# Performance work log

Measured on AMD Instinct MI355X. Metric: run time of the kernel, lower is better.

## Reference

```python
import jax, jax.numpy as jnp
import numpy as np

BIG = 1e8   # fill value used by to_dense_batch for missing neighbors in the original
EPS_W = 1e-8
EPS_BN = 1e-5


def setup_inputs() -> dict:
    key = jax.random.key(0)
    ks = jax.random.split(key, 8)
    N, S, Dc, Df = 16384, 4096, 256, 64
    fine_xyz = jax.random.normal(ks[0], (1, 3, N), dtype=jnp.float32)
    coarse_xyz = jax.random.normal(ks[1], (1, 3, S), dtype=jnp.float32)
    fine_piece_id = jnp.sort(jax.random.randint(ks[2], (1, 1, N), 0, 4))
    coarse_piece_id = jnp.sort(jax.random.randint(ks[3], (1, 1, S), 0, 4))
    fine_features = jax.random.normal(ks[4], (1, Df, N), dtype=jnp.float32)
    coarse_features = jax.random.normal(ks[5], (1, Dc, S), dtype=jnp.float32)
    # mlp stack: Conv1d(320->256), Conv1d(256->128), each with BatchNorm1d
    W1 = jax.random.normal(ks[6], (256, Dc + Df), dtype=jnp.float32) * 0.05
    b1 = jnp.zeros((256,), jnp.float32)
    g1 = jnp.ones((256,), jnp.float32)
    be1 = jnp.zeros((256,), jnp.float32)
    W2 = jax.random.normal(ks[7], (128, 256), dtype=jnp.float32) * 0.05
    b2 = jnp.zeros((128,), jnp.float32)
    g2 = jnp.ones((128,), jnp.float32)
    be2 = jnp.zeros((128,), jnp.float32)
    return dict(fine_xyz=fine_xyz, coarse_xyz=coarse_xyz,
                fine_piece_id=fine_piece_id, coarse_piece_id=coarse_piece_id,
                fine_features=fine_features, coarse_features=coarse_features,
                W1=W1, b1=b1, g1=g1, be1=be1, W2=W2, b2=b2, g2=g2, be2=be2)


def _bn_relu(x, gamma, beta):
    # x: [N, C]; BatchNorm1d in training mode -> batch stats over the N axis
    mu = jnp.mean(x, axis=0, keepdims=True)
    var = jnp.mean((x - mu) ** 2, axis=0, keepdims=True)  # biased var, as torch BN
    return jax.nn.relu((x - mu) * jax.lax.rsqrt(var + EPS_BN) * gamma + beta)


def reference(fine_xyz, coarse_xyz, fine_piece_id, coarse_piece_id,
              fine_features, coarse_features, W1, b1, g1, be1, W2, b2, g2, be2):
    fxyz = fine_xyz[0].T            # [N, 3]
    cxyz = coarse_xyz[0].T          # [S, 3]
    ff = fine_features[0].T         # [N, Df]
    cf = coarse_features[0].T       # [S, Dc]
    fid = fine_piece_id.reshape(-1)     # [N]
    cid = coarse_piece_id.reshape(-1)   # [S]

    # squared euclidean distances, masked to the same piece (knn with batch vectors)
    d2 = (jnp.sum(fxyz ** 2, -1)[:, None] + jnp.sum(cxyz ** 2, -1)[None, :]
          - 2.0 * fxyz @ cxyz.T)                       # [N, S]
    d2 = jnp.where(fid[:, None] != cid[None, :], BIG, d2)

    neg_d, idx = jax.lax.top_k(-d2, 3)                  # 3-NN per fine point
    dist = -neg_d                                       # [N, 3]

    w = 1.0 / (dist + EPS_W)
    w = w / jnp.sum(w, axis=1, keepdims=True)           # [N, 3]

    gathered = cf[idx]                                  # [N, 3, Dc]
    interp = jnp.sum(gathered * w[:, :, None], axis=1)  # [N, Dc]

    x = jnp.concatenate([interp, ff], axis=-1)          # [N, Dc+Df]
    x = _bn_relu(x @ W1.T + b1, g1, be1)                # [N, 256]
    x = _bn_relu(x @ W2.T + b2, g2, be2)                # [N, 128]
    return x.T[None]                                    # [1, 128, N]
```

## Files before the change

### kernel.cpp

```cpp
#include <hip/hip_runtime.h>
#include <hip/hip_bf16.h>

#define N_FINE   16384
#define S_COARSE 4096
#define DC       256
#define DF       64
#define K1       320
#define C1       256
#define C2       128
#define BIGF     1e8f
#define EPS_W    1e-8f
#define EPS_BN   1e-5f
#define IMAX     0x7fffffff

typedef __attribute__((ext_vector_type(8))) short bf16x8;
typedef __attribute__((ext_vector_type(8))) unsigned short u16x8;
typedef __attribute__((ext_vector_type(4))) float f32x4;

#define OFF_RANGES 0
#define OFF_SUMS   256
#define OFF_SCALE1 3328
#define OFF_SHIFT1 4352
#define OFF_SCALE2 5376
#define OFF_SHIFT2 5888
#define OFF_CPACK  8192
#define OFF_CFT    73728
#define OFF_IDX3   4268032
#define OFF_W3     4464640
#define OFF_W1B    4661248
#define OFF_W2B    4825088
#define OFF_Y1     4890624
#define OFF_Y2     13279232

__device__ inline unsigned short f2bf_bits(float f) {
    __hip_bfloat16 h = __float2bfloat16(f);
    unsigned short u;
    __builtin_memcpy(&u, &h, 2);
    return u;
}
__device__ inline float bf2f(unsigned short u) {
    return __uint_as_float(((unsigned)u) << 16);
}

__global__ __launch_bounds__(256) void setup_kernel(
    const int* __restrict__ cid, int* __restrict__ ranges, float* __restrict__ sums,
    const float* __restrict__ cxyz, float4* __restrict__ cpack,
    const float* __restrict__ W1, const float* __restrict__ W2,
    unsigned short* __restrict__ W1b, unsigned short* __restrict__ W2b,
    const float* __restrict__ cf, float* __restrict__ cfT)
{
    __shared__ float tile[32][33];
    int b = blockIdx.x, t = threadIdx.x;
    if (b == 0) {
        if (t < 8) ranges[t] = 0;
        for (int i = t; i < 768; i += 256) sums[i] = 0.f;
        __syncthreads();
        for (int s = t; s < S_COARSE; s += 256) {
            int c = cid[s];
            if (s == 0 || cid[s - 1] != c) ranges[c] = s;
            if (s == S_COARSE - 1 || cid[s + 1] != c) ranges[4 + c] = s + 1;
        }
    } else if (b <= 16) {
        int s = (b - 1) * 256 + t;
        float x = cxyz[s], y = cxyz[S_COARSE + s], z = cxyz[2 * S_COARSE + s];
        cpack[s] = make_float4(x, y, z, x * x + y * y + z * z);
    } else if (b <= 336) {
        int i = (b - 17) * 256 + t;
        W1b[i] = f2bf_bits(W1[i]);
        if (i < C2 * C1) W2b[i] = f2bf_bits(W2[i]);
    } else {
        int lb = b - 337;
        int tx = t & 31, ty = t >> 5;
        int s0 = (lb & 127) * 32, c0 = (lb >> 7) * 32;
        #pragma unroll
        for (int i = 0; i < 4; i++)
            tile[ty + i * 8][tx] = cf[(c0 + ty + i * 8) * S_COARSE + s0 + tx];
        __syncthreads();
        #pragma unroll
        for (int i = 0; i < 4; i++) {
            int s = ty + i * 8;
            cfT[(s0 + s) * DC + c0 + tx] = tile[tx][s];
        }
    }
}

__global__ __launch_bounds__(256) void knn_kernel(const float* __restrict__ fxyz,
                                                  const int* __restrict__ fpid,
                                                  const float4* __restrict__ cpack,
                                                  const int* __restrict__ ranges,
                                                  int* __restrict__ idx3,
                                                  float* __restrict__ w3) {
    int t = threadIdx.x;
    int lane = t & 63, wid = t >> 6;
    int n = blockIdx.x * 4 + wid;
    int fid = fpid[n];
    float fx = fxyz[n], fy = fxyz[N_FINE + n], fz = fxyz[2 * N_FINE + n];
    float fn2 = fx * fx + fy * fy + fz * fz;
    int st = ranges[fid], en = ranges[4 + fid];

    float d0 = BIGF, d1 = BIGF, d2v = BIGF;
    int i0 = IMAX, i1 = IMAX, i2 = IMAX;
    for (int s = st + lane; s < en; s += 64) {
        float4 c = cpack[s];
        float d = fn2 + c.w - 2.0f * (fx * c.x + fy * c.y + fz * c.z);
        if (d < d0)       { d2v = d1; i2 = i1; d1 = d0; i1 = i0; d0 = d; i0 = s; }
        else if (d < d1)  { d2v = d1; i2 = i1; d1 = d;  i1 = s; }
        else if (d < d2v) { d2v = d;  i2 = s; }
    }
    #pragma unroll
    for (int m = 1; m < 64; m <<= 1) {
        float e0 = __shfl_xor(d0, m, 64), e1 = __shfl_xor(d1, m, 64), e2 = __shfl_xor(d2v, m, 64);
        int   j0 = __shfl_xor(i0, m, 64), j1 = __shfl_xor(i1, m, 64), j2 = __shfl_xor(i2, m, 64);
        #pragma unroll
        for (int q = 0; q < 3; q++) {
            float e = (q == 0) ? e0 : (q == 1) ? e1 : e2;
            int   j = (q == 0) ? j0 : (q == 1) ? j1 : j2;
            bool b0 = (e < d0) || (e == d0 && j < i0);
            bool b1 = (e < d1) || (e == d1 && j < i1);
            bool b2 = (e < d2v) || (e == d2v && j < i2);
            if (b0)      { d2v = d1; i2 = i1; d1 = d0; i1 = i0; d0 = e; i0 = j; }
            else if (b1) { d2v = d1; i2 = i1; d1 = e;  i1 = j; }
            else if (b2) { d2v = e;  i2 = j; }
        }
    }
    if (lane == 0) {
        int cand = 0;
        while (i0 == IMAX || i1 == IMAX || i2 == IMAX) {
            if (cand >= st && cand < en) { cand = en; continue; }
            if (i0 == IMAX)      { i0 = cand; d0 = BIGF; }
            else if (i1 == IMAX) { i1 = cand; d1 = BIGF; }
            else                 { i2 = cand; d2v = BIGF; }
            cand++;
        }
        float w0 = 1.0f / (d0 + EPS_W);
        float w1 = 1.0f / (d1 + EPS_W);
        float w2 = 1.0f / (d2v + EPS_W);
        float inv = 1.0f / (w0 + w1 + w2);
        idx3[n * 3 + 0] = i0; idx3[n * 3 + 1] = i1; idx3[n * 3 + 2] = i2;
        w3[n * 3 + 0] = w0 * inv; w3[n * 3 + 1] = w1 * inv; w3[n * 3 + 2] = w2 * inv;
    }
}

__global__ __launch_bounds__(256) void gemm1_kernel(
    const int* __restrict__ idx3, const float* __restrict__ w3,
    const float* __restrict__ cfT, const float* __restrict__ ff,
    const unsigned short* __restrict__ W1b, const float* __restrict__ bias,
    unsigned short* __restrict__ Y1, float* __restrict__ sums, float* __restrict__ sumsq)
{
    __shared__ __align__(16) unsigned short As[4 * 32 * 8];
    __shared__ __align__(16) unsigned short Bs[4 * 256 * 8];
    __shared__ int   sI[32][3];
    __shared__ float sWt[32][3];
    int t = threadIdx.x;
    int m0 = blockIdx.x * 32;
    int lane = t & 63, wid = t >> 6;
    int wn = wid * 64;

    if (t < 32) {
        sI[t][0]  = idx3[(m0 + t) * 3 + 0];
        sI[t][1]  = idx3[(m0 + t) * 3 + 1];
        sI[t][2]  = idx3[(m0 + t) * 3 + 2];
        sWt[t][0] = w3[(m0 + t) * 3 + 0];
        sWt[t][1] = w3[(m0 + t) * 3 + 1];
        sWt[t][2] = w3[(m0 + t) * 3 + 2];
    }
    int ksA = t & 3, rowA = t >> 2;
    int fxw = ksA << 2;
    int gA = ksA * 32 + (rowA ^ fxw);
    int rowB = t;
    f32x4 acc[2][4] = {};
    int ks = lane >> 4, r16 = lane & 15, fxr = ks << 2;
    __syncthreads();

    const float *c0p = nullptr, *c1p = nullptr, *c2p = nullptr;
    float w0v = 0.f, w1v = 0.f, w2v = 0.f;
    if (t < 128) {
        c0p = &cfT[sI[rowA][0] * DC];
        c1p = &cfT[sI[rowA][1] * DC];
        c2p = &cfT[sI[rowA][2] * DC];
        w0v = sWt[rowA][0]; w1v = sWt[rowA][1]; w2v = sWt[rowA][2];
    }
    const unsigned short* pb = &W1b[(size_t)rowB * K1];

    float r[24];
    u16x8 vb[4];

    {
        int k0 = ksA * 8;
        if (t < 128) {
            *(float4*)&r[0]  = *(const float4*)(c0p + k0);
            *(float4*)&r[4]  = *(const float4*)(c0p + k0 + 4);
            *(float4*)&r[8]  = *(const float4*)(c1p + k0);
            *(float4*)&r[12] = *(const float4*)(c1p + k0 + 4);
            *(float4*)&r[16] = *(const float4*)(c2p + k0);
            *(float4*)&r[20] = *(const float4*)(c2p + k0 + 4);
        }
        #pragma unroll
        for (int kb = 0; kb < 4; kb++) vb[kb] = *(const u16x8*)(pb + kb * 8);
    }

    #pragma unroll
    for (int kt = 0; kt < K1; kt += 32) {
        u16x8 va;
        if (t < 128) {
            int k0 = kt + ksA * 8;
            if (k0 < DC) {
                #pragma unroll
                for (int i = 0; i < 8; i++)
                    va[i] = f2bf_bits(w0v * r[i] + w1v * r[8 + i] + w2v * r[16 + i]);
            } else {
                #pragma unroll
                for (int i = 0; i < 8; i++)
                    va[i] = f2bf_bits(r[i]);
            }
        }
        float rn[24];
        u16x8 vbn[4];
        if (kt + 32 < K1) {
            int k0n = kt + 32 + ksA * 8;
            if (t < 128) {
                if (k0n < DC) {
                    *(float4*)&rn[0]  = *(const float4*)(c0p + k0n);
                    *(float4*)&rn[4]  = *(const float4*)(c0p + k0n + 4);
                    *(float4*)&rn[8]  = *(const float4*)(c1p + k0n);
                    *(float4*)&rn[12] = *(const float4*)(c1p + k0n + 4);
                    *(float4*)&rn[16] = *(const float4*)(c2p + k0n);
                    *(float4*)&rn[20] = *(const float4*)(c2p + k0n + 4);
                } else {
                    int c = k0n - DC;
                    #pragma unroll
                    for (int i = 0; i < 8; i++)
                        rn[i] = ff[(size_t)(c + i) * N_FINE + m0 + rowA];
                }
            }
            #pragma unroll
            for (int kb = 0; kb < 4; kb++)
                vbn[kb] = *(const u16x8*)(pb + kt + 32 + kb * 8);
        }
        __syncthreads();
        if (t < 128) *(u16x8*)&As[gA * 8] = va;
        #pragma unroll
        for (int kb = 0; kb < 4; kb++)
            *(u16x8*)&Bs[(kb * 256 + (rowB ^ (kb << 2))) * 8] = vb[kb];
        __syncthreads();
        bf16x8 af[2], bfr[4];
        #pragma unroll
        for (int mi = 0; mi < 2; mi++)
            af[mi] = *(const bf16x8*)&As[(ks * 32 + ((mi * 16 + r16) ^ fxr)) * 8];
        #pragma unroll
        for (int nj = 0; nj < 4; nj++)
            bfr[nj] = *(const bf16x8*)&Bs[(ks * 256 + ((wn + nj * 16 + r16) ^ fxr)) * 8];
        #pragma unroll
        for (int mi = 0; mi < 2; mi++)
            #pragma unroll
            for (int nj = 0; nj < 4; nj++)
                acc[mi][nj] = __builtin_amdgcn_mfma_f32_16x16x32_bf16(af[mi], bfr[nj], acc[mi][nj], 0, 0, 0);
        if (kt + 32 < K1) {
            #pragma unroll
            for (int i = 0; i < 24; i++) r[i] = rn[i];
            #pragma unroll
            for (int kb = 0; kb < 4; kb++) vb[kb] = vbn[kb];
        }
    }

    float sl[4] = {0.f, 0.f, 0.f, 0.f}, s2l[4] = {0.f, 0.f, 0.f, 0.f};
    #pragma unroll
    for (int nj = 0; nj < 4; nj++) {
        int n = wn + nj * 16 + r16;
        float bb = bias[n];
        #pragma unroll
        for (int mi = 0; mi < 2; mi++) {
            #pragma unroll
            for (int r4 = 0; r4 < 4; r4++) {
                int m = m0 + mi * 16 + ks * 4 + r4;
                float o = acc[mi][nj][r4] + bb;
                Y1[(size_t)m * C1 + n] = f2bf_bits(o);
                sl[nj] += o; s2l[nj] += o * o;
            }
        }
    }
    #pragma unroll
    for (int nj = 0; nj < 4; nj++) {
        sl[nj]  += __shfl_xor(sl[nj],  16, 64);
        sl[nj]  += __shfl_xor(sl[nj],  32, 64);
        s2l[nj] += __shfl_xor(s2l[nj], 16, 64);
        s2l[nj] += __shfl_xor(s2l[nj], 32, 64);
    }
    if (lane < 16) {
        #pragma unroll
        for (int nj = 0; nj < 4; nj++) {
            atomicAdd(&sums[wn + nj * 16 + lane],  sl[nj]);
            atomicAdd(&sumsq[wn + nj * 16 + lane], s2l[nj]);
        }
    }
}

template <int KDIM, int NOUT>
__global__ __launch_bounds__(256) void mfma_gemm2_kernel(
    const unsigned short* __restrict__ A,
    const unsigned short* __restrict__ B,
    const float* __restrict__ bias,
    const float* __restrict__ scale,
    const float* __restrict__ shift,
    float* __restrict__ Yout,
    float* __restrict__ sums, float* __restrict__ sumsq)
{
    __shared__ __align__(16) unsigned short As[4 * 64 * 8];
    __shared__ __align__(16) unsigned short Bs[4 * 64 * 8];
    int t = threadIdx.x;
    int m0 = blockIdx.x * 64, j0 = blockIdx.y * 64;
    int lane = t & 63, wid = t >> 6;
    int wm = (wid >> 1) * 32, wn = (wid & 1) * 32;

    int ksA = t & 3;
    int rowA = t >> 2;
    int fxw = ksA << 2;
    int gA = ksA * 64 + (rowA ^ fxw);
    const unsigned short* pa = A + (size_t)(m0 + rowA) * KDIM + ksA * 8;
    const unsigned short* pb = B + (size_t)(j0 + rowA) * KDIM + ksA * 8;

    f32x4 acc[2][2] = {};
    int ks = lane >> 4, r16 = lane & 15;
    int fxr = ks << 2;

    u16x8 va, vb;
    float4 sc0, sc1, sh0, sh1;
    va = *(const u16x8*)pa;
    vb = *(const u16x8*)pb;
    sc0 = *(const float4*)&scale[ksA * 8];
    sc1 = *(const float4*)&scale[ksA * 8 + 4];
    sh0 = *(const float4*)&shift[ksA * 8];
    sh1 = *(const float4*)&shift[ksA * 8 + 4];

    #pragma unroll
    for (int kt = 0; kt < KDIM; kt += 32) {
        u16x8 vat;
        {
            float scv[8] = {sc0.x, sc0.y, sc0.z, sc0.w, sc1.x, sc1.y, sc1.z, sc1.w};
            float shv[8] = {sh0.x, sh0.y, sh0.z, sh0.w, sh1.x, sh1.y, sh1.z, sh1.w};
            #pragma unroll
            for (int i = 0; i < 8; i++)
                vat[i] = f2bf_bits(fmaxf(fmaf(bf2f(va[i]), scv[i], shv[i]), 0.f));
        }
        u16x8 van, vbn;
        float4 sc0n, sc1n, sh0n, sh1n;
        if (kt + 32 < KDIM) {
            van = *(const u16x8*)(pa + kt + 32);
            vbn = *(const u16x8*)(pb + kt + 32);
            int kb = kt + 32 + ksA * 8;
            sc0n = *(const float4*)&scale[kb];
            sc1n = *(const float4*)&scale[kb + 4];
            sh0n = *(const float4*)&shift[kb];
            sh1n = *(const float4*)&shift[kb + 4];
        }
        __syncthreads();
        *(u16x8*)&As[gA * 8] = vat;
        *(u16x8*)&Bs[gA * 8] = vb;
        __syncthreads();
        bf16x8 af[2], bfr[2];
        #pragma unroll
        for (int mi = 0; mi < 2; mi++)
            af[mi] = *(const bf16x8*)&As[(ks * 64 + ((wm + mi * 16 + r16) ^ fxr)) * 8];
        #pragma unroll
        for (int nj = 0; nj < 2; nj++)
            bfr[nj] = *(const bf16x8*)&Bs[(ks * 64 + ((wn + nj * 16 + r16) ^ fxr)) * 8];
        #pragma unroll
        for (int mi = 0; mi < 2; mi++)
            #pragma unroll
            for (int nj = 0; nj < 2; nj++)
                acc[mi][nj] = __builtin_amdgcn_mfma_f32_16x16x32_bf16(af[mi], bfr[nj], acc[mi][nj], 0, 0, 0);
        if (kt + 32 < KDIM) {
            va = van; vb = vbn;
            sc0 = sc0n; sc1 = sc1n; sh0 = sh0n; sh1 = sh1n;
        }
    }

    float sl[2] = {0.f, 0.f}, s2l[2] = {0.f, 0.f};
    #pragma unroll
    for (int nj = 0; nj < 2; nj++) {
        int n = j0 + wn + nj * 16 + r16;
        float bb = bias[n];
        #pragma unroll
        for (int mi = 0; mi < 2; mi++) {
            #pragma unroll
            for (int r4 = 0; r4 < 4; r4++) {
                int m = m0 + wm + mi * 16 + ks * 4 + r4;
                float o = acc[mi][nj][r4] + bb;
                Yout[(size_t)m * NOUT + n] = o;
                sl[nj] += o; s2l[nj] += o * o;
            }
        }
    }
    #pragma unroll
    for (int nj = 0; nj < 2; nj++) {
        sl[nj]  += __shfl_xor(sl[nj],  16, 64);
        sl[nj]  += __shfl_xor(sl[nj],  32, 64);
        s2l[nj] += __shfl_xor(s2l[nj], 16, 64);
        s2l[nj] += __shfl_xor(s2l[nj], 32, 64);
    }
    if (lane < 16) {
        atomicAdd(&sums[j0 + wn + lane],       sl[0]);
        atomicAdd(&sums[j0 + wn + 16 + lane],  sl[1]);
        atomicAdd(&sumsq[j0 + wn + lane],      s2l[0]);
        atomicAdd(&sumsq[j0 + wn + 16 + lane], s2l[1]);
    }
}

__global__ void finalize_kernel(const float* __restrict__ sums, const float* __restrict__ sumsq,
                                const float* __restrict__ g, const float* __restrict__ be,
                                float* __restrict__ scale, float* __restrict__ shift, int C) {
    int t = threadIdx.x;
    if (t < C) {
        float mean = sums[t] * (1.0f / N_FINE);
        float var = sumsq[t] * (1.0f / N_FINE) - mean * mean;
        float sc = g[t] * rsqrtf(var + EPS_BN);
        scale[t] = sc;
        shift[t] = be[t] - mean * sc;
    }
}

__global__ __launch_bounds__(256) void out_kernel(const float* __restrict__ Y2,
                                                  const float* __restrict__ scale2,
                                                  const float* __restrict__ shift2,
                                                  float* __restrict__ out) {
    __shared__ float tile[64][65];
    int t = threadIdx.x;
    int n0 = blockIdx.x * 64, c0 = blockIdx.y * 64;
    int cl = t & 63, rg = t >> 6;
    #pragma unroll
    for (int i = 0; i < 16; i++) {
        int r = rg + i * 4;
        tile[r][cl] = Y2[(n0 + r) * C2 + c0 + cl];
    }
    __syncthreads();
    #pragma unroll
    for (int i = 0; i < 16; i++) {
        int c = rg + i * 4;
        float v = fmaf(tile[cl][c], scale2[c0 + c], shift2[c0 + c]);
        out[(c0 + c) * N_FINE + n0 + cl] = fmaxf(v, 0.f);
    }
}

extern "C" void kernel_launch(void* const* d_in, const int* in_sizes, int n_in,
                              void* d_out, int out_size, void* d_ws, size_t ws_size,
                              hipStream_t stream) {
    const float* fine_xyz   = (const float*)d_in[0];
    const float* coarse_xyz = (const float*)d_in[1];
    const int*   fine_pid   = (const int*)d_in[2];
    const int*   coarse_pid = (const int*)d_in[3];
    const float* fine_feat  = (const float*)d_in[4];
    const float* coarse_feat= (const float*)d_in[5];
    const float* W1  = (const float*)d_in[6];
    const float* b1  = (const float*)d_in[7];
    const float* g1  = (const float*)d_in[8];
    const float* be1 = (const float*)d_in[9];
    const float* W2  = (const float*)d_in[10];
    const float* b2  = (const float*)d_in[11];
    const float* g2  = (const float*)d_in[12];
    const float* be2 = (const float*)d_in[13];
    float* out = (float*)d_out;

    char* ws = (char*)d_ws;
    int*    ranges = (int*)(ws + OFF_RANGES);
    float*  sums1  = (float*)(ws + OFF_SUMS);
    float*  sumsq1 = sums1 + 256;
    float*  sums2  = sums1 + 512;
    float*  sumsq2 = sums1 + 640;
    float*  scale1 = (float*)(ws + OFF_SCALE1);
    float*  shift1 = (float*)(ws + OFF_SHIFT1);
    float*  scale2 = (float*)(ws + OFF_SCALE2);
    float*  shift2 = (float*)(ws + OFF_SHIFT2);
    float4* cpack  = (float4*)(ws + OFF_CPACK);
    float*  cfT    = (float*)(ws + OFF_CFT);
    int*    idx3   = (int*)(ws + OFF_IDX3);
    float*  w3     = (float*)(ws + OFF_W3);
    unsigned short* W1b = (unsigned short*)(ws + OFF_W1B);
    unsigned short* W2b = (unsigned short*)(ws + OFF_W2B);
    unsigned short* Y1  = (unsigned short*)(ws + OFF_Y1);
    float*          Y2  = (float*)(ws + OFF_Y2);

    setup_kernel<<<1361, 256, 0, stream>>>(coarse_pid, ranges, sums1,
                                           coarse_xyz, cpack, W1, W2, W1b, W2b,
                                           coarse_feat, cfT);
    knn_kernel<<<N_FINE / 4, 256, 0, stream>>>(fine_xyz, fine_pid, cpack, ranges, idx3, w3);

    gemm1_kernel<<<N_FINE / 32, 256, 0, stream>>>(idx3, w3, cfT, fine_feat,
                                                  W1b, b1, Y1, sums1, sumsq1);
    finalize_kernel<<<1, 256, 0, stream>>>(sums1, sumsq1, g1, be1, scale1, shift1, C1);

    mfma_gemm2_kernel<C1, C2><<<dim3(N_FINE / 64, C2 / 64), 256, 0, stream>>>(
        Y1, W2b, b2, scale1, shift1, Y2, sums2, sumsq2);
    finalize_kernel<<<1, 256, 0, stream>>>(sums2, sumsq2, g2, be2, scale2, shift2, C2);

    out_kernel<<<dim3(N_FINE / 64, C2 / 64), 256, 0, stream>>>(Y2, scale2, shift2, out);
}
```

Baseline: 180.6 us.

## Fuse kNN search into GEMM1 and fold BN finalize into consumer kernels

The separate kNN kernel is removed. Each GEMM1 block now finds the 3 nearest coarse points for its own 32 rows, one wavefront per 8 points, and writes indices and weights straight into shared memory. The two single-block finalize kernels are also removed: GEMM2 and the output kernel compute BN scale and shift from the sums at their start. This drops three launches and the idx3/w3 round trip through global memory. In exchange, each GEMM1 block runs the kNN scans serially before its matmul, and every consumer block recomputes the BN parameters.

New measurement: 203.8 us. 1.13x slower.

```diff
diff --git a/kernel.cpp b/kernel.cpp
--- a/kernel.cpp
+++ b/kernel.cpp
@@ -19,18 +19,12 @@
 
 #define OFF_RANGES 0
 #define OFF_SUMS   256
-#define OFF_SCALE1 3328
-#define OFF_SHIFT1 4352
-#define OFF_SCALE2 5376
-#define OFF_SHIFT2 5888
 #define OFF_CPACK  8192
 #define OFF_CFT    73728
-#define OFF_IDX3   4268032
-#define OFF_W3     4464640
-#define OFF_W1B    4661248
-#define OFF_W2B    4825088
-#define OFF_Y1     4890624
-#define OFF_Y2     13279232
+#define OFF_W1B    4268032
+#define OFF_W2B    4431872
+#define OFF_Y1     4497408
+#define OFF_Y2     12886016
 
 __device__ inline unsigned short f2bf_bits(float f) {
     __hip_bfloat16 h = __float2bfloat16(f);
@@ -84,65 +78,9 @@
     }
 }
 
-__global__ __launch_bounds__(256) void knn_kernel(const float* __restrict__ fxyz,
-                                                  const int* __restrict__ fpid,
-                                                  const float4* __restrict__ cpack,
-                                                  const int* __restrict__ ranges,
-                                                  int* __restrict__ idx3,
-                                                  float* __restrict__ w3) {
-    int t = threadIdx.x;
-    int lane = t & 63, wid = t >> 6;
-    int n = blockIdx.x * 4 + wid;
-    int fid = fpid[n];
-    float fx = fxyz[n], fy = fxyz[N_FINE + n], fz = fxyz[2 * N_FINE + n];
-    float fn2 = fx * fx + fy * fy + fz * fz;
-    int st = ranges[fid], en = ranges[4 + fid];
-
-    float d0 = BIGF, d1 = BIGF, d2v = BIGF;
-    int i0 = IMAX, i1 = IMAX, i2 = IMAX;
-    for (int s = st + lane; s < en; s += 64) {
-        float4 c = cpack[s];
-        float d = fn2 + c.w - 2.0f * (fx * c.x + fy * c.y + fz * c.z);
-        if (d < d0)       { d2v = d1; i2 = i1; d1 = d0; i1 = i0; d0 = d; i0 = s; }
-        else if (d < d1)  { d2v = d1; i2 = i1; d1 = d;  i1 = s; }
-        else if (d < d2v) { d2v = d;  i2 = s; }
-    }
-    #pragma unroll
-    for (int m = 1; m < 64; m <<= 1) {
-        float e0 = __shfl_xor(d0, m, 64), e1 = __shfl_xor(d1, m, 64), e2 = __shfl_xor(d2v, m, 64);
-        int   j0 = __shfl_xor(i0, m, 64), j1 = __shfl_xor(i1, m, 64), j2 = __shfl_xor(i2, m, 64);
-        #pragma unroll
-        for (int q = 0; q < 3; q++) {
-            float e = (q == 0) ? e0 : (q == 1) ? e1 : e2;
-            int   j = (q == 0) ? j0 : (q == 1) ? j1 : j2;
-            bool b0 = (e < d0) || (e == d0 && j < i0);
-            bool b1 = (e < d1) || (e == d1 && j < i1);
-            bool b2 = (e < d2v) || (e == d2v && j < i2);
-            if (b0)      { d2v = d1; i2 = i1; d1 = d0; i1 = i0; d0 = e; i0 = j; }
-            else if (b1) { d2v = d1; i2 = i1; d1 = e;  i1 = j; }
-            else if (b2) { d2v = e;  i2 = j; }
-        }
-    }
-    if (lane == 0) {
-        int cand = 0;
-        while (i0 == IMAX || i1 == IMAX || i2 == IMAX) {
-            if (cand >= st && cand < en) { cand = en; continue; }
-            if (i0 == IMAX)      { i0 = cand; d0 = BIGF; }
-            else if (i1 == IMAX) { i1 = cand; d1 = BIGF; }
-            else                 { i2 = cand; d2v = BIGF; }
-            cand++;
-        }
-        float w0 = 1.0f / (d0 + EPS_W);
-        float w1 = 1.0f / (d1 + EPS_W);
-        float w2 = 1.0f / (d2v + EPS_W);
-        float inv = 1.0f / (w0 + w1 + w2);
-        idx3[n * 3 + 0] = i0; idx3[n * 3 + 1] = i1; idx3[n * 3 + 2] = i2;
-        w3[n * 3 + 0] = w0 * inv; w3[n * 3 + 1] = w1 * inv; w3[n * 3 + 2] = w2 * inv;
-    }
-}
-
 __global__ __launch_bounds__(256) void gemm1_kernel(
-    const int* __restrict__ idx3, const float* __restrict__ w3,
+    const float* __restrict__ fxyz, const int* __restrict__ fpid,
+    const float4* __restrict__ cpack, const int* __restrict__ ranges,
     const float* __restrict__ cfT, const float* __restrict__ ff,
     const unsigned short* __restrict__ W1b, const float* __restrict__ bias,
     unsigned short* __restrict__ Y1, float* __restrict__ sums, float* __restrict__ sumsq)
@@ -156,21 +94,63 @@
     int lane = t & 63, wid = t >> 6;
     int wn = wid * 64;
 
-    if (t < 32) {
-        sI[t][0]  = idx3[(m0 + t) * 3 + 0];
-        sI[t][1]  = idx3[(m0 + t) * 3 + 1];
-        sI[t][2]  = idx3[(m0 + t) * 3 + 2];
-        sWt[t][0] = w3[(m0 + t) * 3 + 0];
-        sWt[t][1] = w3[(m0 + t) * 3 + 1];
-        sWt[t][2] = w3[(m0 + t) * 3 + 2];
-    }
+    for (int pp = 0; pp < 8; ++pp) {
+        int p = wid * 8 + pp;
+        int n = m0 + p;
+        int fid = fpid[n];
+        float fx = fxyz[n], fy = fxyz[N_FINE + n], fz = fxyz[2 * N_FINE + n];
+        float fn2 = fx * fx + fy * fy + fz * fz;
+        int st = ranges[fid], en = ranges[4 + fid];
+        float d0 = BIGF, d1 = BIGF, d2v = BIGF;
+        int i0 = IMAX, i1 = IMAX, i2 = IMAX;
+        for (int s = st + lane; s < en; s += 64) {
+            float4 c = cpack[s];
+            float d = fn2 + c.w - 2.0f * (fx * c.x + fy * c.y + fz * c.z);
+            if (d < d0)       { d2v = d1; i2 = i1; d1 = d0; i1 = i0; d0 = d; i0 = s; }
+            else if (d < d1)  { d2v = d1; i2 = i1; d1 = d;  i1 = s; }
+            else if (d < d2v) { d2v = d;  i2 = s; }
+        }
+        #pragma unroll
+        for (int m = 1; m < 64; m <<= 1) {
+            float e0 = __shfl_xor(d0, m, 64), e1 = __shfl_xor(d1, m, 64), e2 = __shfl_xor(d2v, m, 64);
+            int   j0 = __shfl_xor(i0, m, 64), j1 = __shfl_xor(i1, m, 64), j2 = __shfl_xor(i2, m, 64);
+            #pragma unroll
+            for (int q = 0; q < 3; q++) {
+                float e = (q == 0) ? e0 : (q == 1) ? e1 : e2;
+                int   j = (q == 0) ? j0 : (q == 1) ? j1 : j2;
+                bool b0 = (e < d0) || (e == d0 && j < i0);
+                bool b1 = (e < d1) || (e == d1 && j < i1);
+                bool b2 = (e < d2v) || (e == d2v && j < i2);
+                if (b0)      { d2v = d1; i2 = i1; d1 = d0; i1 = i0; d0 = e; i0 = j; }
+                else if (b1) { d2v = d1; i2 = i1; d1 = e;  i1 = j; }
+                else if (b2) { d2v = e;  i2 = j; }
+            }
+        }
+        if (lane == 0) {
+            int cand = 0;
+            while (i0 == IMAX || i1 == IMAX || i2 == IMAX) {
+                if (cand >= st && cand < en) { cand = en; continue; }
+                if (i0 == IMAX)      { i0 = cand; d0 = BIGF; }
+                else if (i1 == IMAX) { i1 = cand; d1 = BIGF; }
+                else                 { i2 = cand; d2v = BIGF; }
+                cand++;
+            }
+            float w0 = 1.0f / (d0 + EPS_W);
+            float w1 = 1.0f / (d1 + EPS_W);
+            float w2 = 1.0f / (d2v + EPS_W);
+            float inv = 1.0f / (w0 + w1 + w2);
+            sI[p][0] = i0; sI[p][1] = i1; sI[p][2] = i2;
+            sWt[p][0] = w0 * inv; sWt[p][1] = w1 * inv; sWt[p][2] = w2 * inv;
+        }
+    }
+    __syncthreads();
+
     int ksA = t & 3, rowA = t >> 2;
     int fxw = ksA << 2;
     int gA = ksA * 32 + (rowA ^ fxw);
     int rowB = t;
     f32x4 acc[2][4] = {};
     int ks = lane >> 4, r16 = lane & 15, fxr = ks << 2;
-    __syncthreads();
 
     const float *c0p = nullptr, *c1p = nullptr, *c2p = nullptr;
     float w0v = 0.f, w1v = 0.f, w2v = 0.f;
@@ -184,7 +164,6 @@
 
     float r[24];
     u16x8 vb[4];
-
     {
         int k0 = ksA * 8;
         if (t < 128) {
@@ -300,17 +279,26 @@
     const unsigned short* __restrict__ A,
     const unsigned short* __restrict__ B,
     const float* __restrict__ bias,
-    const float* __restrict__ scale,
-    const float* __restrict__ shift,
+    const float* __restrict__ sums1, const float* __restrict__ sumsq1,
+    const float* __restrict__ g1, const float* __restrict__ be1,
     float* __restrict__ Yout,
     float* __restrict__ sums, float* __restrict__ sumsq)
 {
     __shared__ __align__(16) unsigned short As[4 * 64 * 8];
     __shared__ __align__(16) unsigned short Bs[4 * 64 * 8];
+    __shared__ float sSc[KDIM], sSh[KDIM];
     int t = threadIdx.x;
     int m0 = blockIdx.x * 64, j0 = blockIdx.y * 64;
     int lane = t & 63, wid = t >> 6;
     int wm = (wid >> 1) * 32, wn = (wid & 1) * 32;
+
+    {
+        float mean = sums1[t] * (1.0f / N_FINE);
+        float var = sumsq1[t] * (1.0f / N_FINE) - mean * mean;
+        float sc = g1[t] * rsqrtf(var + EPS_BN);
+        sSc[t] = sc;
+        sSh[t] = be1[t] - mean * sc;
+    }
 
     int ksA = t & 3;
     int rowA = t >> 2;
@@ -323,35 +311,23 @@
     int ks = lane >> 4, r16 = lane & 15;
     int fxr = ks << 2;
 
-    u16x8 va, vb;
-    float4 sc0, sc1, sh0, sh1;
-    va = *(const u16x8*)pa;
-    vb = *(const u16x8*)pb;
-    sc0 = *(const float4*)&scale[ksA * 8];
-    sc1 = *(const float4*)&scale[ksA * 8 + 4];
-    sh0 = *(const float4*)&shift[ksA * 8];
-    sh1 = *(const float4*)&shift[ksA * 8 + 4];
+    u16x8 va = *(const u16x8*)pa;
+    u16x8 vb = *(const u16x8*)pb;
+    __syncthreads();
 
     #pragma unroll
     for (int kt = 0; kt < KDIM; kt += 32) {
         u16x8 vat;
         {
-            float scv[8] = {sc0.x, sc0.y, sc0.z, sc0.w, sc1.x, sc1.y, sc1.z, sc1.w};
-            float shv[8] = {sh0.x, sh0.y, sh0.z, sh0.w, sh1.x, sh1.y, sh1.z, sh1.w};
+            int kb = kt + ksA * 8;
             #pragma unroll
             for (int i = 0; i < 8; i++)
-                vat[i] = f2bf_bits(fmaxf(fmaf(bf2f(va[i]), scv[i], shv[i]), 0.f));
+                vat[i] = f2bf_bits(fmaxf(fmaf(bf2f(va[i]), sSc[kb + i], sSh[kb + i]), 0.f));
         }
         u16x8 van, vbn;
-        float4 sc0n, sc1n, sh0n, sh1n;
         if (kt + 32 < KDIM) {
             van = *(const u16x8*)(pa + kt + 32);
             vbn = *(const u16x8*)(pb + kt + 32);
-            int kb = kt + 32 + ksA * 8;
-            sc0n = *(const float4*)&scale[kb];
-            sc1n = *(const float4*)&scale[kb + 4];
-            sh0n = *(const float4*)&shift[kb];
-            sh1n = *(const float4*)&shift[kb + 4];
         }
         __syncthreads();
         *(u16x8*)&As[gA * 8] = vat;
@@ -369,10 +345,7 @@
             #pragma unroll
             for (int nj = 0; nj < 2; nj++)
                 acc[mi][nj] = __builtin_amdgcn_mfma_f32_16x16x32_bf16(af[mi], bfr[nj], acc[mi][nj], 0, 0, 0);
-        if (kt + 32 < KDIM) {
-            va = van; vb = vbn;
-            sc0 = sc0n; sc1 = sc1n; sh0 = sh0n; sh1 = sh1n;
-        }
+        if (kt + 32 < KDIM) { va = van; vb = vbn; }
     }
 
     float sl[2] = {0.f, 0.f}, s2l[2] = {0.f, 0.f};
@@ -406,26 +379,24 @@
     }
 }
 
-__global__ void finalize_kernel(const float* __restrict__ sums, const float* __restrict__ sumsq,
-                                const float* __restrict__ g, const float* __restrict__ be,
-                                float* __restrict__ scale, float* __restrict__ shift, int C) {
-    int t = threadIdx.x;
-    if (t < C) {
-        float mean = sums[t] * (1.0f / N_FINE);
-        float var = sumsq[t] * (1.0f / N_FINE) - mean * mean;
-        float sc = g[t] * rsqrtf(var + EPS_BN);
-        scale[t] = sc;
-        shift[t] = be[t] - mean * sc;
-    }
-}
-
 __global__ __launch_bounds__(256) void out_kernel(const float* __restrict__ Y2,
-                                                  const float* __restrict__ scale2,
-                                                  const float* __restrict__ shift2,
+                                                  const float* __restrict__ sums2,
+                                                  const float* __restrict__ sumsq2,
+                                                  const float* __restrict__ g2,
+                                                  const float* __restrict__ be2,
                                                   float* __restrict__ out) {
     __shared__ float tile[64][65];
+    __shared__ float sSc[64], sSh[64];
     int t = threadIdx.x;
     int n0 = blockIdx.x * 64, c0 = blockIdx.y * 64;
+    if (t < 64) {
+        int c = c0 + t;
+        float mean = sums2[c] * (1.0f / N_FINE);
+        float var = sumsq2[c] * (1.0f / N_FINE) - mean * mean;
+        float sc = g2[c] * rsqrtf(var + EPS_BN);
+        sSc[t] = sc;
+        sSh[t] = be2[c] - mean * sc;
+    }
     int cl = t & 63, rg = t >> 6;
     #pragma unroll
     for (int i = 0; i < 16; i++) {
@@ -436,7 +407,7 @@
     #pragma unroll
     for (int i = 0; i < 16; i++) {
         int c = rg + i * 4;
-        float v = fmaf(tile[cl][c], scale2[c0 + c], shift2[c0 + c]);
+        float v = fmaf(tile[cl][c], sSc[c], sSh[c]);
         out[(c0 + c) * N_FINE + n0 + cl] = fmaxf(v, 0.f);
     }
 }
@@ -466,14 +437,8 @@
     float*  sumsq1 = sums1 + 256;
     float*  sums2  = sums1 + 512;
     float*  sumsq2 = sums1 + 640;
-    float*  scale1 = (float*)(ws + OFF_SCALE1);
-    float*  shift1 = (float*)(ws + OFF_SHIFT1);
-    float*  scale2 = (float*)(ws + OFF_SCALE2);
-    float*  shift2 = (float*)(ws + OFF_SHIFT2);
     float4* cpack  = (float4*)(ws + OFF_CPACK);
     float*  cfT    = (float*)(ws + OFF_CFT);
-    int*    idx3   = (int*)(ws + OFF_IDX3);
-    float*  w3     = (float*)(ws + OFF_W3);
     unsigned short* W1b = (unsigned short*)(ws + OFF_W1B);
     unsigned short* W2b = (unsigned short*)(ws + OFF_W2B);
     unsigned short* Y1  = (unsigned short*)(ws + OFF_Y1);
@@ -482,15 +447,14 @@
     setup_kernel<<<1361, 256, 0, stream>>>(coarse_pid, ranges, sums1,
                                            coarse_xyz, cpack, W1, W2, W1b, W2b,
                                            coarse_feat, cfT);
-    knn_kernel<<<N_FINE / 4, 256, 0, stream>>>(fine_xyz, fine_pid, cpack, ranges, idx3, w3);
-
-    gemm1_kernel<<<N_FINE / 32, 256, 0, stream>>>(idx3, w3, cfT, fine_feat,
-                                                  W1b, b1, Y1, sums1, sumsq1);
-    finalize_kernel<<<1, 256, 0, stream>>>(sums1, sumsq1, g1, be1, scale1, shift1, C1);
+
+    gemm1_kernel<<<N_FINE / 32, 256, 0, stream>>>(fine_xyz, fine_pid, cpack, ranges,
+                                                  cfT, fine_feat, W1b, b1,
+                                                  Y1, sums1, sumsq1);
 
     mfma_gemm2_kernel<C1, C2><<<dim3(N_FINE / 64, C2 / 64), 256, 0, stream>>>(
-        Y1, W2b, b2, scale1, shift1, Y2, sums2, sumsq2);
-    finalize_kernel<<<1, 256, 0, stream>>>(sums2, sumsq2, g2, be2, scale2, shift2, C2);
-
-    out_kernel<<<dim3(N_FINE / 64, C2 / 64), 256, 0, stream>>>(Y2, scale2, shift2, out);
-}
+        Y1, W2b, b2, sums1, sumsq1, g1, be1, Y2, sums2, sumsq2);
+
+    out_kernel<<<dim3(N_FINE / 64, C2 / 64), 256, 0, stream>>>(Y2, sums2, sumsq2,
+                                                               g2, be2, out);
+}
```
